# Kernel tuning notes

Measured on AMD Instinct MI355X. Metric: run time of the kernel, lower is better.

Reference implementation:

```python
import jax, jax.numpy as jnp
import numpy as np

B, S, D, H = 1, 4096, 768, 12
HD = D // H
FF = 4 * D
EPS = 1e-5


def _layer_norm(x, w, b):
    mu = jnp.mean(x, axis=-1, keepdims=True)
    var = jnp.mean((x - mu) ** 2, axis=-1, keepdims=True)
    return (x - mu) * jax.lax.rsqrt(var + EPS) * w + b


def setup_inputs() -> dict:
    key = jax.random.key(0)
    ks = jax.random.split(key, 16)
    s = 0.02
    inp = {
        "hidden_states": jax.random.normal(ks[0], (B, S, D), jnp.float32),
        "attention_mask": jnp.ones((B, S), jnp.int32),
        "ln1_w": jnp.ones((D,), jnp.float32),
        "ln1_b": jnp.zeros((D,), jnp.float32),
        "wq": jax.random.normal(ks[1], (D, D), jnp.float32) * s,
        "bq": jnp.zeros((D,), jnp.float32),
        "wk": jax.random.normal(ks[2], (D, D), jnp.float32) * s,
        "bk": jnp.zeros((D,), jnp.float32),
        "wv": jax.random.normal(ks[3], (D, D), jnp.float32) * s,
        "bv": jnp.zeros((D,), jnp.float32),
        "wo": jax.random.normal(ks[4], (D, D), jnp.float32) * s,
        "bo": jnp.zeros((D,), jnp.float32),
        "ln2_w": jnp.ones((D,), jnp.float32),
        "ln2_b": jnp.zeros((D,), jnp.float32),
        "w_up": jax.random.normal(ks[5], (D, FF), jnp.float32) * s,
        "b_up": jnp.zeros((FF,), jnp.float32),
        "w_down": jax.random.normal(ks[6], (FF, D), jnp.float32) * s,
        "b_down": jnp.zeros((D,), jnp.float32),
    }
    return inp


def reference(hidden_states, attention_mask, ln1_w, ln1_b, wq, bq, wk, bk, wv, bv,
              wo, bo, ln2_w, ln2_b, w_up, b_up, w_down, b_down):
    b, s, _ = hidden_states.shape
    residual = hidden_states
    x = _layer_norm(hidden_states, ln1_w, ln1_b)
    # projections; weights stored [in, out]
    q = (x @ wq + bq).reshape(b, s, H, HD).transpose(0, 2, 1, 3)  # (b,h,s,hd)
    k = (x @ wk + bk).reshape(b, s, H, HD).transpose(0, 2, 1, 3)
    v = (x @ wv + bv).reshape(b, s, H, HD).transpose(0, 2, 1, 3)
    scores = jnp.einsum("bhqd,bhkd->bhqk", q, k) / np.float32(np.sqrt(HD))
    causal = jnp.triu(jnp.ones((s, s), bool), k=1)  # True above diagonal -> mask
    neg_inf = jnp.float32(-jnp.inf)
    scores = jnp.where(causal[None, None, :, :], neg_inf, scores)
    pad = (attention_mask[:, None, None, :] == 0)
    scores = jnp.where(pad, neg_inf, scores)
    weights = jax.nn.softmax(scores, axis=-1)
    attn = jnp.einsum("bhqk,bhkd->bhqd", weights, v)
    attn = attn.transpose(0, 2, 1, 3).reshape(b, s, D)
    hidden = residual + (attn @ wo + bo)
    # FFN
    residual = hidden
    y = _layer_norm(hidden, ln2_w, ln2_b)
    y = jax.nn.gelu(y @ w_up + b_up, approximate=False)
    y = y @ w_down + b_down
    return residual + y
```

## Files before the change

### kernel.cpp

```cpp
#include <hip/hip_runtime.h>
#include <cstdint>
#include <cstddef>


#define S_  4096
#define D_  768
#define H_  12
#define HD_ 64
#define FF_ 3072
#define SD_ (4096 * 768)

typedef short  short8  __attribute__((ext_vector_type(8)));
typedef float  floatx4 __attribute__((ext_vector_type(4)));

__device__ __forceinline__ float bf2f(unsigned short h) {
  union { unsigned int u; float f; } v; v.u = ((unsigned int)h) << 16; return v.f;
}
__device__ __forceinline__ unsigned short f2bf(float f) {
  union { unsigned int u; float f; } v; v.f = f;
  unsigned int u = v.u;
  return (unsigned short)((u + 0x7FFFu + ((u >> 16) & 1u)) >> 16);
}
__device__ __forceinline__ unsigned int cvt_pk_bf16(float lo, float hi) {
  unsigned int r;
  asm("v_cvt_pk_bf16_f32 %0, %1, %2" : "=v"(r) : "v"(lo), "v"(hi));
  return r;
}
__device__ __forceinline__ void gload_lds16(const unsigned short* g, unsigned short* l) {
  __builtin_amdgcn_global_load_lds(
      (const __attribute__((address_space(1))) unsigned int*)g,
      (__attribute__((address_space(3))) unsigned int*)l, 16, 0, 0);
}

__global__ void k_cvt_f32(const void* __restrict__ src, float* __restrict__ dst,
                          int n, const int* __restrict__ flagp) {
  const int flag = *flagp;
  for (int i = blockIdx.x * blockDim.x + threadIdx.x; i < n; i += gridDim.x * blockDim.x)
    dst[i] = flag ? ((const float*)src)[i] : bf2f(((const unsigned short*)src)[i]);
}

__global__ __launch_bounds__(256) void k_cvt_t6(
    const void* s0, const void* s1, const void* s2, const void* s3,
    const void* s4, const void* s5,
    unsigned short* d0, unsigned short* d1, unsigned short* d2,
    unsigned short* d3, unsigned short* d4, unsigned short* d5,
    const int* __restrict__ flagp) {
  __shared__ unsigned short T[64 * 65];
  const int flag = *flagp;
  const int b = blockIdx.x;
  const void* src; unsigned short* dst; int K, N, ti;
  if (b < 576) {
    const int seg = b / 144; ti = b - seg * 144; K = 768; N = 768;
    const void* ss[4] = {s0, s1, s2, s3};
    unsigned short* dd[4] = {d0, d1, d2, d3};
    src = ss[seg]; dst = dd[seg];
  } else if (b < 1152) { ti = b - 576;  K = 768;  N = 3072; src = s4; dst = d4; }
  else                 { ti = b - 1152; K = 3072; N = 768;  src = s5; dst = d5; }
  const int nx = N >> 6;
  const int n0 = (ti % nx) * 64, k0 = (ti / nx) * 64;
  const int t = threadIdx.x;
  const int cl = t & 63, rg = t >> 6;
#pragma unroll
  for (int i = 0; i < 16; ++i) {
    const int kl = rg * 16 + i;
    const size_t si = (size_t)(k0 + kl) * N + n0 + cl;
    T[kl * 65 + cl] = flag ? f2bf(((const float*)src)[si]) : ((const unsigned short*)src)[si];
  }
  __syncthreads();
#pragma unroll
  for (int i = 0; i < 16; ++i) {
    const int nl = rg * 16 + i;
    dst[(size_t)(n0 + nl) * K + k0 + cl] = T[cl * 65 + nl];
  }
}

__global__ void k_cvt_params(const void* p0, const void* p1, const void* p2, const void* p3,
                             const void* p4, const void* p5, const void* p6, const void* p7,
                             const void* p8, const void* p9,
                             float* __restrict__ dst, int* __restrict__ flagp) {
  const int flag = (((const unsigned int*)p0)[0] == 0x3F800000u) ? 1 : 0;
  int i = blockIdx.x * 256 + threadIdx.x;
  if (i == 0) *flagp = flag;
  if (i >= 9984) return;
  const void* src; int j;
  if (i < 6912) {
    int seg = i / 768; j = i - seg * 768;
    const void* tbl[9] = {p0, p1, p2, p3, p4, p5, p6, p7, p8};
    src = tbl[seg];
  } else { src = p9; j = i - 6912; }
  dst[i] = flag ? ((const float*)src)[j] : bf2f(((const unsigned short*)src)[j]);
}

__global__ __launch_bounds__(256) void k_ln(const float* __restrict__ x,
                                            const float* __restrict__ w,
                                            const float* __restrict__ b,
                                            unsigned short* __restrict__ out,
                                            const float* __restrict__ bias2,
                                            float* __restrict__ acc) {
  const int row = blockIdx.x, t = threadIdx.x;
  const float* xr = x + (size_t)row * D_;
  float v0 = xr[t], v1 = xr[t + 256], v2 = xr[t + 512];
  float s = v0 + v1 + v2;
  float ss = v0 * v0 + v1 * v1 + v2 * v2;
  for (int off = 32; off > 0; off >>= 1) {
    s  += __shfl_down(s, off);
    ss += __shfl_down(ss, off);
  }
  __shared__ float sb[4], ssb[4];
  const int wid = t >> 6, lane = t & 63;
  if (lane == 0) { sb[wid] = s; ssb[wid] = ss; }
  __syncthreads();
  s  = sb[0] + sb[1] + sb[2] + sb[3];
  ss = ssb[0] + ssb[1] + ssb[2] + ssb[3];
  const float mu   = s * (1.0f / D_);
  const float var  = ss * (1.0f / D_) - mu * mu;
  const float rstd = rsqrtf(var + 1e-5f);
  unsigned short* orow = out + (size_t)row * D_;
  orow[t]       = f2bf((v0 - mu) * rstd * w[t]       + b[t]);
  orow[t + 256] = f2bf((v1 - mu) * rstd * w[t + 256] + b[t + 256]);
  orow[t + 512] = f2bf((v2 - mu) * rstd * w[t + 512] + b[t + 512]);
  if (acc) {
    float* arow = acc + (size_t)row * D_;
    arow[t]       = v0 + bias2[t];
    arow[t + 256] = v1 + bias2[t + 256];
    arow[t + 512] = v2 + bias2[t + 512];
  }
}

template <int TBM, int TBN>
__global__ __launch_bounds__(256) void k_gemm_t(
    const unsigned short* __restrict__ A, const unsigned short* __restrict__ Wt,
    const float* __restrict__ bias, const float* __restrict__ resid,
    void* __restrict__ Cout, int M, int N, int K, int mode, const int* __restrict__ flagp) {
  constexpr int MI = TBM / 32, MJ = TBN / 32;
  __shared__ __align__(16) unsigned short As[2][TBM * 32];
  __shared__ __align__(16) unsigned short Bs[2][TBN * 32];
  const int t = threadIdx.x;
  const int w = t >> 6, lane = t & 63;
  const int quad = lane >> 4, l16 = lane & 15;

  const int gx = gridDim.x, gy = gridDim.y;
  const int nwg = gx * gy * gridDim.z;
  const int id  = blockIdx.x + gx * (blockIdx.y + gy * blockIdx.z);
  const int v   = (id & 7) * (nwg >> 3) + (id >> 3);
  const int vx  = v % gx;
  const int vyz = v / gx;
  const int vy  = vyz % gy;
  const int vz  = vyz / gy;

  const int mb = vy * TBM, nb = vx * TBN;
  const int wm = (w >> 1) * (TBM / 2), wn = (w & 1) * (TBN / 2);
  const int grow = lane >> 2;
  const int gcol = (lane & 3) * 8;

  floatx4 acc[MI][MJ];
#pragma unroll
  for (int i = 0; i < MI; ++i)
#pragma unroll
    for (int j = 0; j < MJ; ++j) acc[i][j] = (floatx4){0.f, 0.f, 0.f, 0.f};

  const int kpb = K / gridDim.z;
  const int kb0 = kpb * vz;
  const int kend = kb0 + kpb;

  auto stage = [&](int buf, int k0) {
#pragma unroll
    for (int r = 0; r < TBM / 64; ++r) {
      const int ch = r * 4 + w;
      gload_lds16(A + (size_t)(mb + ch * 16 + grow) * K + k0 + gcol, &As[buf][ch * 512]);
    }
#pragma unroll
    for (int r = 0; r < TBN / 64; ++r) {
      const int ch = r * 4 + w;
      gload_lds16(Wt + (size_t)(nb + ch * 16 + grow) * K + k0 + gcol, &Bs[buf][ch * 512]);
    }
  };

  stage(0, kb0);
  asm volatile("s_waitcnt vmcnt(0)" ::: "memory");
  __builtin_amdgcn_s_barrier();

  int cur = 0;
  for (int k0 = kb0; k0 < kend; k0 += 32) {
    if (k0 + 32 < kend) stage(cur ^ 1, k0 + 32);

    union { short8 v; uint4 q; } fa[MI], fb[MJ];
#pragma unroll
    for (int i = 0; i < MI; ++i)
      fa[i].q = *(const uint4*)&As[cur][(wm + i * 16 + l16) * 32 + quad * 8];
#pragma unroll
    for (int j = 0; j < MJ; ++j)
      fb[j].q = *(const uint4*)&Bs[cur][(wn + j * 16 + l16) * 32 + quad * 8];
#pragma unroll
    for (int i = 0; i < MI; ++i)
#pragma unroll
      for (int j = 0; j < MJ; ++j)
        acc[i][j] = __builtin_amdgcn_mfma_f32_16x16x32_bf16(fa[i].v, fb[j].v, acc[i][j], 0, 0, 0);

    asm volatile("s_waitcnt vmcnt(0)" ::: "memory");
    __builtin_amdgcn_s_barrier();
    cur ^= 1;
  }

  const int flag = (mode == 3) ? *flagp : 0;
#pragma unroll
  for (int i = 0; i < MI; ++i) {
#pragma unroll
    for (int j = 0; j < MJ; ++j) {
      const int col = nb + wn + j * 16 + l16;
      const float bv = (mode == 6) ? 0.f : bias[col];
#pragma unroll
      for (int r = 0; r < 4; ++r) {
        const int row = mb + wm + i * 16 + quad * 4 + r;
        const size_t idx = (size_t)row * N + col;
        float v = acc[i][j][r] + bv;
        if (mode == 0) {
          ((unsigned short*)Cout)[idx] = f2bf(v);
        } else if (mode == 1) {
          ((float*)Cout)[idx] = v + resid[idx];
        } else if (mode == 2) {
          float g = 0.5f * v * (1.0f + erff(v * 0.70710678118f));
          ((unsigned short*)Cout)[idx] = f2bf(g);
        } else if (mode == 5) {
          unsigned short* q = (unsigned short*)Cout;
          if (col < 768)        q[(size_t)row * 768 + col] = f2bf(v);
          else if (col < 1536) (q + SD_)[(size_t)row * 768 + col - 768] = f2bf(v);
          else                 (q + 2 * (size_t)SD_)[(size_t)(col - 1536) * 4096 + row] = f2bf(v);
        } else if (mode == 6) {
          unsafeAtomicAdd((float*)Cout + idx, v);
        } else {
          v += resid[idx];
          if (flag) ((float*)Cout)[idx] = v;
          else      ((unsigned short*)Cout)[idx] = f2bf(v);
        }
      }
    }
  }
}

__global__ __launch_bounds__(256) void k_out(const float* __restrict__ acc,
                                             const int* __restrict__ flagp,
                                             void* __restrict__ out) {
  const int i = (blockIdx.x * 256 + threadIdx.x) * 4;
  const floatx4 v = *(const floatx4*)(acc + i);
  if (*flagp) {
    *(floatx4*)((float*)out + i) = v;
  } else {
    union { unsigned short e[4]; uint2 u; } p;
#pragma unroll
    for (int e = 0; e < 4; ++e) p.e[e] = f2bf(v[e]);
    *(uint2*)((unsigned short*)out + i) = p.u;
  }
}

#define LK 72
__global__ __launch_bounds__(256) void k_attn_chunk(
    const unsigned short* __restrict__ qb, const unsigned short* __restrict__ kb,
    const unsigned short* __restrict__ vtb, const int* __restrict__ amask,
    unsigned short* __restrict__ Opart, float* __restrict__ Lpart) {
  const int h = blockIdx.y;
  const int x = 79 - (int)blockIdx.x;
  int g, base;
  if (x < 8)       { g = 0; base = 0; }
  else if (x < 24) { g = 1; base = 8; }
  else if (x < 48) { g = 2; base = 24; }
  else             { g = 3; base = 48; }
  const int rem = x - base;
  const int qt = 8 * g + rem / (g + 1);
  const int c  = rem % (g + 1);
  const int qbase = qt * 128;
  const int kt0 = c * 16;
  const int kt1 = min(kt0 + 16, 2 * qt + 2);

  __shared__ __align__(16) unsigned short Ps[128 * LK];
  const int t = threadIdx.x;
  const int w = t >> 6, lane = t & 63;
  const int quad = lane >> 4, l16 = lane & 15;

  union { short8 v; uint4 q; } qf[2][2];
#pragma unroll
  for (int sub = 0; sub < 2; ++sub) {
    const unsigned short* qp =
        qb + (size_t)(qbase + w * 32 + sub * 16 + l16) * D_ + h * HD_ + quad * 8;
    qf[sub][0].q = *(const uint4*)qp;
    qf[sub][1].q = *(const uint4*)(qp + 32);
  }
  unsigned short* myP = &Ps[w * 32 * LK];

  floatx4 O[2][4];
  float lsum[2] = {0.f, 0.f};
#pragma unroll
  for (int sub = 0; sub < 2; ++sub)
#pragma unroll
    for (int dc = 0; dc < 4; ++dc) O[sub][dc] = (floatx4){0.f, 0.f, 0.f, 0.f};
  const float sscale = 0.125f * 1.4426950408889634f;
  const int qrow0 = qbase + w * 32 + l16;

  for (int kt = kt0; kt < kt1; ++kt) {
    const int kbase = kt * 64;
    const bool diag = (kt >= 2 * qt);

#pragma unroll
    for (int kc = 0; kc < 4; ++kc) {
      union { short8 v; uint4 q; } kf[2];
      const unsigned short* kp =
          kb + (size_t)(kbase + kc * 16 + l16) * D_ + h * HD_ + quad * 8;
      kf[0].q = *(const uint4*)kp;
      kf[1].q = *(const uint4*)(kp + 32);
      floatx4 cc[2];
      __builtin_amdgcn_s_setprio(1);
#pragma unroll
      for (int sub = 0; sub < 2; ++sub) {
        cc[sub] = (floatx4){0.f, 0.f, 0.f, 0.f};
        cc[sub] = __builtin_amdgcn_mfma_f32_16x16x32_bf16(kf[0].v, qf[sub][0].v, cc[sub], 0, 0, 0);
        cc[sub] = __builtin_amdgcn_mfma_f32_16x16x32_bf16(kf[1].v, qf[sub][1].v, cc[sub], 0, 0, 0);
      }
      __builtin_amdgcn_s_setprio(0);
      const int kg0 = kbase + kc * 16 + quad * 4;
      const int4 m4 = *(const int4*)(amask + kg0);
#pragma unroll
      for (int sub = 0; sub < 2; ++sub) {
        const int qr = qrow0 + sub * 16;
        float p[4];
#pragma unroll
        for (int r = 0; r < 4; ++r) {
          const float e = __builtin_amdgcn_exp2f(cc[sub][r] * sscale);
          const int mv = (r == 0) ? m4.x : (r == 1) ? m4.y : (r == 2) ? m4.z : m4.w;
          const bool keep = (mv != 0) && (!diag || (kg0 + r <= qr));
          p[r] = keep ? e : 0.f;
          lsum[sub] += p[r];
        }
        const unsigned int d0 = cvt_pk_bf16(p[0], p[1]);
        const unsigned int d1 = cvt_pk_bf16(p[2], p[3]);
        *(uint2*)&myP[(sub * 16 + l16) * LK + kc * 16 + quad * 4] = (uint2){d0, d1};
      }
    }

    union { short8 v; uint4 q; } pf[2][2];
#pragma unroll
    for (int sub = 0; sub < 2; ++sub) {
      const unsigned short* p0 = &myP[(sub * 16 + l16) * LK + quad * 8];
      pf[sub][0].q = *(const uint4*)p0;
      pf[sub][1].q = *(const uint4*)(p0 + 32);
    }
#pragma unroll
    for (int dc = 0; dc < 4; ++dc) {
      union { short8 v; uint4 q; } vf[2];
      const unsigned short* vp =
          vtb + (size_t)(h * HD_ + dc * 16 + l16) * S_ + kbase + quad * 8;
      vf[0].q = *(const uint4*)vp;
      vf[1].q = *(const uint4*)(vp + 32);
      __builtin_amdgcn_s_setprio(1);
#pragma unroll
      for (int sub = 0; sub < 2; ++sub) {
        O[sub][dc] = __builtin_amdgcn_mfma_f32_16x16x32_bf16(pf[sub][0].v, vf[0].v, O[sub][dc], 0, 0, 0);
        O[sub][dc] = __builtin_amdgcn_mfma_f32_16x16x32_bf16(pf[sub][1].v, vf[1].v, O[sub][dc], 0, 0, 0);
      }
      __builtin_amdgcn_s_setprio(0);
    }
  }

#pragma unroll
  for (int sub = 0; sub < 2; ++sub) {
    lsum[sub] += __shfl_xor(lsum[sub], 16);
    lsum[sub] += __shfl_xor(lsum[sub], 32);
  }

  const size_t slot = (size_t)h * 80 + x;
#pragma unroll
  for (int sub = 0; sub < 2; ++sub) {
#pragma unroll
    for (int dc = 0; dc < 4; ++dc)
#pragma unroll
      for (int r = 0; r < 4; ++r)
        Opart[slot * 8192 + (w * 32 + sub * 16 + quad * 4 + r) * 64 + dc * 16 + l16] =
            f2bf(O[sub][dc][r]);
    if (lane < 16)
      Lpart[slot * 128 + w * 32 + sub * 16 + lane] = lsum[sub];
  }
}

__global__ __launch_bounds__(256) void k_attn_merge(
    const unsigned short* __restrict__ Opart, const float* __restrict__ Lpart,
    unsigned short* __restrict__ ob) {
  const int qt = blockIdx.x, h = blockIdx.y;
  const int t = threadIdx.x;
  const int row = t >> 1, half = (t & 1) * 32;
  const int g = qt >> 3;
  const int nch = g + 1;
  const int cb = h * 80 + 4 * g * (g + 1) + (qt & 7) * (g + 1);
  float L = 0.f;
  float acc[32];
#pragma unroll
  for (int j = 0; j < 32; ++j) acc[j] = 0.f;
  for (int ci = 0; ci < nch; ++ci) {
    L += Lpart[(size_t)(cb + ci) * 128 + row];
    const unsigned short* op = Opart + (size_t)(cb + ci) * 8192 + row * 64 + half;
#pragma unroll
    for (int j4 = 0; j4 < 4; ++j4) {
      union { uint4 v; unsigned short e[8]; } u;
      u.v = *(const uint4*)(op + j4 * 8);
#pragma unroll
      for (int e = 0; e < 8; ++e) acc[j4 * 8 + e] += bf2f(u.e[e]);
    }
  }
  const float inv = 1.f / L;
  unsigned short* orow = ob + (size_t)(qt * 128 + row) * D_ + h * HD_ + half;
#pragma unroll
  for (int j4 = 0; j4 < 4; ++j4) {
    union { uint4 v; unsigned short e[8]; } u;
#pragma unroll
    for (int e = 0; e < 8; ++e) u.e[e] = f2bf(acc[j4 * 8 + e] * inv);
    *(uint4*)(orow + j4 * 8) = u.v;
  }
}

extern "C" void kernel_launch(void* const* d_in, const int* in_sizes, int n_in,
                              void* d_out, int out_size, void* d_ws, size_t ws_size,
                              hipStream_t stream) {
  const void* hidden = d_in[0];
  const int*  amask  = (const int*)d_in[1];
  const void* ln1w = d_in[2];  const void* ln1b = d_in[3];
  const void* wq   = d_in[4];  const void* bq   = d_in[5];
  const void* wk   = d_in[6];  const void* bk   = d_in[7];
  const void* wv   = d_in[8];  const void* bv   = d_in[9];
  const void* wo   = d_in[10]; const void* bo   = d_in[11];
  const void* ln2w = d_in[12]; const void* ln2b = d_in[13];
  const void* wup  = d_in[14]; const void* bup  = d_in[15];
  const void* wdn  = d_in[16]; const void* bdn  = d_in[17];

  char* ws = (char*)d_ws;
  size_t off = 0;
  auto alloc = [&](size_t bytes) {
    char* p = ws + off;
    off += (bytes + 255) & ~(size_t)255;
    return p;
  };
  const size_t SD = (size_t)SD_;
  int*            flagp = (int*)alloc(4);
  float*          h1    = (float*)alloc(SD * 4);
  float*          prm   = (float*)alloc(9984 * 4);
  float*          h2    = (float*)alloc(SD * 4);
  unsigned short* xb    = (unsigned short*)alloc(SD * 2);
  unsigned short* wqkvt = (unsigned short*)alloc((size_t)2304 * 768 * 2);
  unsigned short* wot   = (unsigned short*)alloc((size_t)768 * 768 * 2);
  unsigned short* wupt  = (unsigned short*)alloc((size_t)3072 * 768 * 2);
  unsigned short* wdnt  = (unsigned short*)alloc((size_t)768 * 3072 * 2);
  unsigned short* big   = (unsigned short*)alloc((size_t)S_ * FF_ * 2);
  unsigned short* qb2 = big;
  unsigned short* kb2 = big + SD;
  unsigned short* vtb = big + 2 * SD;
  unsigned short* ab  = big + 3 * SD;
  unsigned short* ffb = big;
  unsigned short* Opart = (unsigned short*)h2;
  float*          Lpart = (float*)((char*)h2 + (size_t)960 * 8192 * 2);

  float* f_ln1w = prm;        float* f_ln1b = prm + 768;
  float* f_ln2w = prm + 1536; float* f_ln2b = prm + 2304;
  float* f_bqkv = prm + 3072; float* f_bo = prm + 5376;
  float* f_bdn = prm + 6144;  float* f_bup = prm + 6912;

  k_cvt_params<<<39, 256, 0, stream>>>(ln1w, ln1b, ln2w, ln2b, bq, bk, bv, bo, bdn, bup,
                                       prm, flagp);
  k_cvt_f32<<<1024, 256, 0, stream>>>(hidden, h1, (int)SD, flagp);
  k_cvt_t6<<<1728, 256, 0, stream>>>(wq, wk, wv, wo, wup, wdn,
                                     wqkvt, wqkvt + 768 * 768, wqkvt + 2 * 768 * 768,
                                     wot, wupt, wdnt, flagp);

  k_ln<<<S_, 256, 0, stream>>>(h1, f_ln1w, f_ln1b, xb, nullptr, nullptr);

  k_gemm_t<128, 128><<<dim3(18, 32), 256, 0, stream>>>(
      xb, wqkvt, f_bqkv, nullptr, qb2, S_, 2304, 768, 5, flagp);

  k_attn_chunk<<<dim3(80, 12), 256, 0, stream>>>(qb2, kb2, vtb, amask, Opart, Lpart);
  k_attn_merge<<<dim3(32, 12), 256, 0, stream>>>(Opart, Lpart, ab);

  k_gemm_t<128, 64><<<dim3(12, 32), 256, 0, stream>>>(
      ab, wot, f_bo, h1, h2, S_, 768, 768, 1, flagp);

  k_ln<<<S_, 256, 0, stream>>>(h2, f_ln2w, f_ln2b, xb, f_bdn, h1);

  k_gemm_t<128, 128><<<dim3(24, 32), 256, 0, stream>>>(
      xb, wupt, f_bup, nullptr, ffb, S_, 3072, 768, 2, flagp);

  k_gemm_t<128, 128><<<dim3(6, 32, 4), 256, 0, stream>>>(
      ffb, wdnt, nullptr, nullptr, h1, S_, 768, 3072, 6, flagp);

  k_out<<<3072, 256, 0, stream>>>(h1, flagp, d_out);
}
```

Measured before the change: 453.1 us.

## Stage K/V tiles in shared memory with register prefetch in attention kernel

The attention chunk kernel now loads each 64-key K and V^T tile cooperatively into LDS once per block, instead of every wave reading them separately from global memory. The next tile is prefetched into registers while the current one is being computed, and the mask slice is also staged in LDS. This cuts redundant global/L2 traffic across the 4 waves and hides load latency. In exchange it adds two __syncthreads per iteration and more LDS use, which may lower occupancy.

```diff
diff --git a/kernel.cpp b/kernel.cpp
--- a/kernel.cpp
+++ b/kernel.cpp
@@ -272,10 +272,14 @@
   const int kt0 = c * 16;
   const int kt1 = min(kt0 + 16, 2 * qt + 2);
 
+  __shared__ __align__(16) unsigned short Kt[64 * LK];
+  __shared__ __align__(16) unsigned short Vt[64 * LK];
   __shared__ __align__(16) unsigned short Ps[128 * LK];
+  __shared__ int Mk[64];
   const int t = threadIdx.x;
   const int w = t >> 6, lane = t & 63;
   const int quad = lane >> 4, l16 = lane & 15;
+  const int sr = t >> 2, sc = (t & 3) * 16;
 
   union { short8 v; uint4 q; } qf[2][2];
 #pragma unroll
@@ -294,19 +298,39 @@
 #pragma unroll
     for (int dc = 0; dc < 4; ++dc) O[sub][dc] = (floatx4){0.f, 0.f, 0.f, 0.f};
   const float sscale = 0.125f * 1.4426950408889634f;
-  const int qrow0 = qbase + w * 32 + l16;
+  const int qcol0 = qbase + w * 32 + l16;
+
+  uint4 kr0, kr1, vr0, vr1; int mreg = 0;
+  auto prefetch = [&](int kt) {
+    const int kbase = kt * 64;
+    const unsigned short* ks = kb + (size_t)(kbase + sr) * D_ + h * HD_ + sc;
+    kr0 = *(const uint4*)ks;
+    kr1 = *(const uint4*)(ks + 8);
+    const unsigned short* vs = vtb + (size_t)(h * HD_ + sr) * S_ + kbase + sc;
+    vr0 = *(const uint4*)vs;
+    vr1 = *(const uint4*)(vs + 8);
+    if (t < 64) mreg = amask[kbase + t];
+  };
+  prefetch(kt0);
 
   for (int kt = kt0; kt < kt1; ++kt) {
     const int kbase = kt * 64;
+    *(uint4*)&Kt[sr * LK + sc]     = kr0;
+    *(uint4*)&Kt[sr * LK + sc + 8] = kr1;
+    *(uint4*)&Vt[sr * LK + sc]     = vr0;
+    *(uint4*)&Vt[sr * LK + sc + 8] = vr1;
+    if (t < 64) Mk[t] = mreg;
+    __syncthreads();
+
+    if (kt + 1 < kt1) prefetch(kt + 1);
+
     const bool diag = (kt >= 2 * qt);
-
 #pragma unroll
     for (int kc = 0; kc < 4; ++kc) {
       union { short8 v; uint4 q; } kf[2];
-      const unsigned short* kp =
-          kb + (size_t)(kbase + kc * 16 + l16) * D_ + h * HD_ + quad * 8;
-      kf[0].q = *(const uint4*)kp;
-      kf[1].q = *(const uint4*)(kp + 32);
+      const unsigned short* p0 = &Kt[(kc * 16 + l16) * LK + quad * 8];
+      kf[0].q = *(const uint4*)p0;
+      kf[1].q = *(const uint4*)(p0 + 32);
       floatx4 cc[2];
       __builtin_amdgcn_s_setprio(1);
 #pragma unroll
@@ -316,11 +340,12 @@
         cc[sub] = __builtin_amdgcn_mfma_f32_16x16x32_bf16(kf[1].v, qf[sub][1].v, cc[sub], 0, 0, 0);
       }
       __builtin_amdgcn_s_setprio(0);
-      const int kg0 = kbase + kc * 16 + quad * 4;
-      const int4 m4 = *(const int4*)(amask + kg0);
+      const int kl0 = kc * 16 + quad * 4;
+      const int kg0 = kbase + kl0;
+      const int4 m4 = *(const int4*)&Mk[kl0];
 #pragma unroll
       for (int sub = 0; sub < 2; ++sub) {
-        const int qr = qrow0 + sub * 16;
+        const int qr = qcol0 + sub * 16;
         float p[4];
 #pragma unroll
         for (int r = 0; r < 4; ++r) {
@@ -332,7 +357,7 @@
         }
         const unsigned int d0 = cvt_pk_bf16(p[0], p[1]);
         const unsigned int d1 = cvt_pk_bf16(p[2], p[3]);
-        *(uint2*)&myP[(sub * 16 + l16) * LK + kc * 16 + quad * 4] = (uint2){d0, d1};
+        *(uint2*)&myP[(sub * 16 + l16) * LK + kl0] = (uint2){d0, d1};
       }
     }
 
@@ -343,21 +368,21 @@
       pf[sub][0].q = *(const uint4*)p0;
       pf[sub][1].q = *(const uint4*)(p0 + 32);
     }
+    __builtin_amdgcn_s_setprio(1);
 #pragma unroll
     for (int dc = 0; dc < 4; ++dc) {
       union { short8 v; uint4 q; } vf[2];
-      const unsigned short* vp =
-          vtb + (size_t)(h * HD_ + dc * 16 + l16) * S_ + kbase + quad * 8;
-      vf[0].q = *(const uint4*)vp;
-      vf[1].q = *(const uint4*)(vp + 32);
-      __builtin_amdgcn_s_setprio(1);
+      const unsigned short* p0 = &Vt[(dc * 16 + l16) * LK + quad * 8];
+      vf[0].q = *(const uint4*)p0;
+      vf[1].q = *(const uint4*)(p0 + 32);
 #pragma unroll
       for (int sub = 0; sub < 2; ++sub) {
         O[sub][dc] = __builtin_amdgcn_mfma_f32_16x16x32_bf16(pf[sub][0].v, vf[0].v, O[sub][dc], 0, 0, 0);
         O[sub][dc] = __builtin_amdgcn_mfma_f32_16x16x32_bf16(pf[sub][1].v, vf[1].v, O[sub][dc], 0, 0, 0);
       }
-      __builtin_amdgcn_s_setprio(0);
-    }
+    }
+    __builtin_amdgcn_s_setprio(0);
+    __syncthreads();
   }
 
 #pragma unroll
```

Result: slower. 464.6 us (+2.6%).
